# Kernel optimization log

Measured on AMD Instinct MI355X. Metric: run time of the kernel, lower is better.

## Reference

```python
import jax, jax.numpy as jnp
import numpy as np

B, H, M, K = 256, 1024, 20, 20  # batch, hidden, max_ingr, pairing top_k (must be equal: M==K)
VOCAB, INGR_V = 32000, 5000


def setup_inputs() -> dict:
    key = jax.random.key(0)
    ks = jax.random.split(key, 24)
    s = 0.02
    inp = {
        "input_ids": jax.random.randint(ks[0], (1, B), 0, VOCAB),
        "hidden": jax.random.normal(ks[1], (1, B, H), jnp.float32),
        "encoder_outputs": jax.random.normal(ks[2], (M, B, 2 * H), jnp.float32),
        "input_tensor": jax.random.randint(ks[3], (B, M), 0, INGR_V),
        "pairing_ids": jax.random.randint(ks[4], (INGR_V, K), 0, INGR_V),
        # parameters
        "emb_dec": jax.random.normal(ks[5], (VOCAB, H), jnp.float32) * s,
        "enc_emb": jax.random.normal(ks[6], (INGR_V, 2 * H), jnp.float32) * s,
        "Wq_i": jax.random.normal(ks[7], (H, H), jnp.float32) * s,
        "Wk_i": jax.random.normal(ks[8], (2 * H, H), jnp.float32) * s,
        "wa_i": jax.random.normal(ks[9], (H,), jnp.float32) * s,
        "Wq_p": jax.random.normal(ks[10], (H, H), jnp.float32) * s,
        "Wk_p": jax.random.normal(ks[11], (2 * H, H), jnp.float32) * s,
        "wa_p": jax.random.normal(ks[12], (H,), jnp.float32) * s,
        "ba_p": jax.random.normal(ks[13], (), jnp.float32) * s,
        "W_lin": jax.random.normal(ks[14], (3 * H, 2 * H), jnp.float32) * s,
        "b_lin": jnp.zeros((2 * H,), jnp.float32),
        "W_ih": jax.random.normal(ks[15], (3 * H, 2 * H), jnp.float32) * s,
        "W_hh": jax.random.normal(ks[16], (3 * H, H), jnp.float32) * s,
        "b_ih": jnp.zeros((3 * H,), jnp.float32),
        "b_hh": jnp.zeros((3 * H,), jnp.float32),
        "W_out": jax.random.normal(ks[17], (H, VOCAB), jnp.float32) * s,
        "b_out": jnp.zeros((VOCAB,), jnp.float32),
    }
    return inp


def reference(input_ids, hidden, encoder_outputs, input_tensor, pairing_ids,
              emb_dec, enc_emb, Wq_i, Wk_i, wa_i, Wq_p, Wk_p, wa_p, ba_p,
              W_lin, b_lin, W_ih, W_hh, b_ih, b_hh, W_out, b_out):
    h = hidden[0]                              # (B, H)
    emb = jnp.take(emb_dec, input_ids[0], axis=0)  # (B, H)

    # ---- IngrAtt (additive attention over ingredients) ----
    # torch code does a raw .view(B, M, 2H) on a (M, B, 2H) tensor -> plain reshape
    enc = encoder_outputs.reshape(B, M, 2 * H)
    query = h @ Wq_i                           # (B, H)
    key = enc @ Wk_i                           # (B, M, H)
    scores_i = jnp.tanh(query[:, None, :] + key) @ wa_i  # (B, M)
    aw = jax.nn.softmax(scores_i, axis=-1)     # (B, M)

    # ---- retrieval: pick most-attended ingredient, gather its top-k pairings ----
    ingr_arg = jnp.argmax(aw, axis=1)                          # (B,)
    ingr_id = input_tensor[jnp.arange(B), ingr_arg]            # (B,)
    comp_ids = jnp.take(pairing_ids, ingr_id, axis=0)          # (B, K)
    comp_emb = jnp.take(enc_emb, comp_ids, axis=0)             # (B, K, 2H)

    # ---- PairingAtt ----
    q_p = h @ Wq_p                             # (B, H)
    k_p = comp_emb @ Wk_p                      # (B, K, H)
    s_p = jnp.tanh(q_p[:, None, :] + k_p) @ wa_p + ba_p  # (B, K)
    a_p = jax.nn.softmax(s_p, axis=-1)
    attn_scores = a_p * s_p                    # (B, K) softmax-weighted raw scores
    attn_app = jnp.einsum('bk,bkd->bd', attn_scores, comp_emb)  # (B, 2H)

    out_pair = jnp.concatenate([emb, attn_app], axis=-1)  # (B, 3H)
    x = out_pair @ W_lin + b_lin                           # (B, 2H) -> GRU input

    # ---- single GRU step (torch gate ordering r,z,n) ----
    gi = x @ W_ih.T + b_ih
    gh = h @ W_hh.T + b_hh
    i_r, i_z, i_n = jnp.split(gi, 3, axis=-1)
    h_r, h_z, h_n = jnp.split(gh, 3, axis=-1)
    r = jax.nn.sigmoid(i_r + h_r)
    z = jax.nn.sigmoid(i_z + h_z)
    n = jnp.tanh(i_n + r * h_n)
    h_new = (1.0 - z) * n + z * h              # (B, H)

    logits = h_new @ W_out + b_out             # (B, VOCAB)
    return logits
```

## Files before the change

### kernel.cpp

```cpp
#include <hip/hip_runtime.h>
#include <cstdio>


using f32x4   = __attribute__((ext_vector_type(4))) float;
using bf16x8  = __attribute__((ext_vector_type(8))) short;
using ushort8 = __attribute__((ext_vector_type(8))) unsigned short;

__device__ __forceinline__ unsigned short f2bf(float x) {
    unsigned u = __builtin_bit_cast(unsigned, x);
    u += 0x7fffu + ((u >> 16) & 1u);
    return (unsigned short)(u >> 16);
}
__device__ __forceinline__ float bf2f(unsigned short u) {
    return __builtin_bit_cast(float, ((unsigned)u) << 16);
}

__device__ __forceinline__ void gload16(const void* g, void* l) {
    auto gp = (const __attribute__((address_space(1))) void*)g;
    auto lp = (__attribute__((address_space(3))) void*)l;
    __builtin_amdgcn_global_load_lds(gp, lp, 16, 0, 0);
}

__device__ __forceinline__ void transpose_body(
    const float* __restrict__ in, unsigned short* __restrict__ out,
    int R, int C, int r0, int c0)
{
    __shared__ float t[32][129];
    const int tid = threadIdx.x;
    const int lr = tid >> 3;
    const int cc = (tid & 7) * 4;
    #pragma unroll
    for (int i = 0; i < 4; ++i) {
        int r = lr + 32 * i;
        float4 v = *(const float4*)(in + (size_t)(r0 + r) * C + c0 + cc);
        t[cc + 0][r] = v.x; t[cc + 1][r] = v.y;
        t[cc + 2][r] = v.z; t[cc + 3][r] = v.w;
    }
    __syncthreads();
    const int rc = (tid & 15) * 8;
    #pragma unroll
    for (int p = 0; p < 2; ++p) {
        int c = (tid >> 4) + 16 * p;
        const float* src = &t[c][rc];
        ushort8 o;
        #pragma unroll
        for (int j = 0; j < 8; ++j) o[j] = f2bf(src[j]);
        *(ushort8*)(out + (size_t)(c0 + c) * R + r0 + rc) = o;
    }
}

__global__ __launch_bounds__(256) void prep1_kernel(
    const float* __restrict__ hidden, const float* __restrict__ enc_out,
    const float* __restrict__ enc_emb,
    const float* __restrict__ Wq_i, const float* __restrict__ Wq_p,
    const float* __restrict__ Wk_i, const float* __restrict__ Wk_p,
    unsigned short* __restrict__ hb, unsigned short* __restrict__ encb,
    unsigned short* __restrict__ encembb,
    unsigned short* __restrict__ WqiT, unsigned short* __restrict__ WqpT,
    unsigned short* __restrict__ WkiT, unsigned short* __restrict__ WkpT)
{
    const int bid = blockIdx.x;
    if (bid < 20496) {
        int i = bid * 256 + threadIdx.x;
        const float* src; unsigned short* dst; int j;
        if (i < 65536)        { src = hidden;  dst = hb;      j = i; }
        else if (i < 2686976) { src = enc_out; dst = encb;    j = i - 65536; }
        else                  { src = enc_emb; dst = encembb; j = i - 2686976; }
        float4 v = ((const float4*)src)[j];
        ((ushort4*)dst)[j] = make_ushort4(f2bf(v.x), f2bf(v.y), f2bf(v.z), f2bf(v.w));
    } else if (bid < 21008) {
        int local = bid - 20496;
        int bz = local >> 8, rem = local & 255;
        transpose_body(bz ? Wq_p : Wq_i, bz ? WqpT : WqiT,
                       1024, 1024, (rem >> 5) * 128, (rem & 31) * 32);
    } else {
        int local = bid - 21008;
        int bz = local >> 9, rem = local & 511;
        transpose_body(bz ? Wk_p : Wk_i, bz ? WkpT : WkiT,
                       2048, 1024, (rem >> 5) * 128, (rem & 31) * 32);
    }
}

template<int OUTBF, bool HAS_BIAS>
__device__ __forceinline__ void gemm_core(
    const unsigned short* __restrict__ A, const unsigned short* __restrict__ Bt,
    const float* __restrict__ bias, void* __restrict__ Cout, int Ncols,
    int sA, int sB, int kLen, int m0, int n0,
    unsigned short* lA, unsigned short* lB)
{
    const int tid = threadIdx.x;
    const int lane = tid & 63, wave = tid >> 6;
    const int wr = wave >> 1, wc = wave & 1;
    const int srow = tid >> 3, schunk = tid & 7;
    const int lm = lane & 15, lk = (lane >> 4) * 8;

    f32x4 acc[4][4];
    #pragma unroll
    for (int m = 0; m < 4; ++m)
        #pragma unroll
        for (int n = 0; n < 4; ++n) { f32x4 z = {0.f,0.f,0.f,0.f}; acc[m][n] = z; }

    const unsigned short* Ag = A  + (size_t)(m0 + srow) * sA + schunk * 8;
    const unsigned short* Bg = Bt + (size_t)(n0 + srow) * sB + schunk * 8;
    const int nt = kLen >> 6;

    char* lap = (char*)lA + tid * 16;
    char* lbp = (char*)lB + tid * 16;

    for (int t = 0; t < nt; ++t) {
        #pragma unroll
        for (int i = 0; i < 4; ++i) {
            gload16(Ag + (size_t)(32 * i) * sA + t * 64, lap + i * 4096);
            gload16(Bg + (size_t)(32 * i) * sB + t * 64, lbp + i * 4096);
        }
        __syncthreads();
        #pragma unroll
        for (int kk = 0; kk < 2; ++kk) {
            bf16x8 af[4], bv[4];
            #pragma unroll
            for (int m = 0; m < 4; ++m)
                af[m] = *(const bf16x8*)((const char*)lA +
                          (wr * 64 + m * 16 + lm) * 128 + (kk * 32 + lk) * 2);
            #pragma unroll
            for (int n = 0; n < 4; ++n)
                bv[n] = *(const bf16x8*)((const char*)lB +
                          (wc * 64 + n * 16 + lm) * 128 + (kk * 32 + lk) * 2);
            #pragma unroll
            for (int m = 0; m < 4; ++m)
                #pragma unroll
                for (int n = 0; n < 4; ++n)
                    acc[m][n] = __builtin_amdgcn_mfma_f32_16x16x32_bf16(
                        af[m], bv[n], acc[m][n], 0, 0, 0);
        }
        __syncthreads();
    }

    const int rbase = m0 + wr * 64 + (lane >> 4) * 4;
    const int cbase = n0 + wc * 64 + lm;
    #pragma unroll
    for (int m = 0; m < 4; ++m) {
        #pragma unroll
        for (int n = 0; n < 4; ++n) {
            int col = cbase + n * 16;
            float bvv = HAS_BIAS ? bias[col] : 0.0f;
            #pragma unroll
            for (int j = 0; j < 4; ++j) {
                int row = rbase + m * 16 + j;
                float v = acc[m][n][j] + bvv;
                if (OUTBF)
                    ((unsigned short*)Cout)[(size_t)row * Ncols + col] = f2bf(v);
                else
                    ((float*)Cout)[(size_t)row * Ncols + col] = v;
            }
        }
    }
}

#define GEMM_SHARED \
    __shared__ unsigned short lA[8192]; __shared__ unsigned short lB[8192];

__global__ __launch_bounds__(256) void gemm_dual_kernel(
    const unsigned short* A, const unsigned short* B0, const unsigned short* B1,
    float* P0, float* P1)
{
    GEMM_SHARED
    const int g = blockIdx.z >> 2, s = blockIdx.z & 3;
    const unsigned short* Bt = (g ? B1 : B0) + s * 256;
    float* C = (g ? P1 : P0) + (size_t)s * 262144;
    gemm_core<0,false>(A + s * 256, Bt, nullptr, C, 1024, 1024, 1024, 256,
                       blockIdx.y * 128, blockIdx.x * 128, lA, lB);
}

__global__ __launch_bounds__(256) void gemm24p_kernel(
    const unsigned short* encembb, const unsigned short* encb,
    const unsigned short* WkpT, const unsigned short* WkiT,
    unsigned short* kpP, unsigned short* keyP, size_t pStride)
{
    __shared__ unsigned short lA0[4096]; __shared__ unsigned short lA1[4096];
    __shared__ unsigned short lB0[4096]; __shared__ unsigned short lB1[4096];
    const int w   = (int)blockIdx.x;
    const int xcd = w & 7;
    const int r   = w >> 3;
    const int z   = xcd >> 1;
    const int by  = (xcd & 1) * 20 + (r >> 3);
    const int bx  = r & 7;
    const int g = z >> 1, h = z & 1;
    const unsigned short* A  = (g ? encb : encembb) + h * 1024;
    const unsigned short* Bt = (g ? WkiT : WkpT)    + h * 1024;
    unsigned short* Cb = (g ? keyP : kpP) + (size_t)h * pStride;
    const int m0 = by * 128, n0 = bx * 128;
    const int tid = threadIdx.x;
    const int lane = tid & 63, wave = tid >> 6;
    const int wr = wave >> 1, wc = wave & 1;
    const int lm = lane & 15;
    const int q  = lane >> 4;
    const int srow = tid >> 2;
    const int sc   = (tid & 3) ^ (srow & 3);

    f32x4 acc[4][4];
    #pragma unroll
    for (int m = 0; m < 4; ++m)
        #pragma unroll
        for (int n = 0; n < 4; ++n) { f32x4 zz = {0.f,0.f,0.f,0.f}; acc[m][n] = zz; }

    const unsigned short* Ag = A  + (size_t)(m0 + srow) * 2048 + sc * 8;
    const unsigned short* Bg = Bt + (size_t)(n0 + srow) * 2048 + sc * 8;

    auto stage = [&](unsigned short* la_, unsigned short* lb_, int t) {
        char* pa = (char*)la_ + tid * 16;
        char* pb = (char*)lb_ + tid * 16;
        gload16(Ag + t * 32, pa);
        gload16(Ag + (size_t)64 * 2048 + t * 32, pa + 4096);
        gload16(Bg + t * 32, pb);
        gload16(Bg + (size_t)64 * 2048 + t * 32, pb + 4096);
    };
    auto compute = [&](const unsigned short* la_, const unsigned short* lb_) {
        bf16x8 af[4], bv[4];
        #pragma unroll
        for (int m = 0; m < 4; ++m) {
            int rr = wr * 64 + m * 16 + lm;
            af[m] = *(const bf16x8*)((const char*)la_ + rr * 64 + ((q ^ (rr & 3)) * 16));
        }
        #pragma unroll
        for (int n = 0; n < 4; ++n) {
            int rr = wc * 64 + n * 16 + lm;
            bv[n] = *(const bf16x8*)((const char*)lb_ + rr * 64 + ((q ^ (rr & 3)) * 16));
        }
        #pragma unroll
        for (int m = 0; m < 4; ++m)
            #pragma unroll
            for (int n = 0; n < 4; ++n)
                acc[m][n] = __builtin_amdgcn_mfma_f32_16x16x32_bf16(
                    af[m], bv[n], acc[m][n], 0, 0, 0);
    };

    stage(lA0, lB0, 0);
    stage(lA1, lB1, 1);
    asm volatile("s_waitcnt vmcnt(4)" ::: "memory");
    __builtin_amdgcn_s_barrier();
    __builtin_amdgcn_sched_barrier(0);

    for (int t = 0; t < 30; t += 2) {
        compute(lA0, lB0);
        __builtin_amdgcn_s_barrier();
        __builtin_amdgcn_sched_barrier(0);
        stage(lA0, lB0, t + 2);
        asm volatile("s_waitcnt vmcnt(4)" ::: "memory");
        __builtin_amdgcn_s_barrier();
        __builtin_amdgcn_sched_barrier(0);

        compute(lA1, lB1);
        __builtin_amdgcn_s_barrier();
        __builtin_amdgcn_sched_barrier(0);
        stage(lA1, lB1, t + 3);
        asm volatile("s_waitcnt vmcnt(4)" ::: "memory");
        __builtin_amdgcn_s_barrier();
        __builtin_amdgcn_sched_barrier(0);
    }
    compute(lA0, lB0);
    asm volatile("s_waitcnt vmcnt(0)" ::: "memory");
    __builtin_amdgcn_s_barrier();
    __builtin_amdgcn_sched_barrier(0);
    compute(lA1, lB1);

    const int rbase = m0 + wr * 64 + q * 4;
    const int cbase = n0 + wc * 64 + lm;
    #pragma unroll
    for (int m = 0; m < 4; ++m)
        #pragma unroll
        for (int n = 0; n < 4; ++n)
            #pragma unroll
            for (int j = 0; j < 4; ++j)
                Cb[(size_t)(rbase + m * 16 + j) * 1024 + cbase + n * 16] =
                    f2bf(acc[m][n][j]);
}

__global__ __launch_bounds__(256) void attn_scores2q_kernel(
    const float* __restrict__ pqQ, const unsigned short* __restrict__ kP,
    size_t kStride, const float* __restrict__ wa, float* __restrict__ scores)
{
    const int bm = blockIdx.x;
    const int b  = bm / 20;
    const int tid = threadIdx.x;
    float4 qa = ((const float4*)(pqQ + (size_t)b * 1024))[tid];
    float4 qb = ((const float4*)(pqQ + 262144 + (size_t)b * 1024))[tid];
    float4 qc = ((const float4*)(pqQ + 524288 + (size_t)b * 1024))[tid];
    float4 qd = ((const float4*)(pqQ + 786432 + (size_t)b * 1024))[tid];
    float4 qv = make_float4(qa.x + qb.x + qc.x + qd.x, qa.y + qb.y + qc.y + qd.y,
                            qa.z + qb.z + qc.z + qd.z, qa.w + qb.w + qc.w + qd.w);
    ushort4 k0 = ((const ushort4*)(kP + (size_t)bm * 1024))[tid];
    ushort4 k1 = ((const ushort4*)(kP + kStride + (size_t)bm * 1024))[tid];
    float4 wv  = ((const float4*)wa)[tid];
    float p = tanhf(qv.x + bf2f(k0.x) + bf2f(k1.x)) * wv.x
            + tanhf(qv.y + bf2f(k0.y) + bf2f(k1.y)) * wv.y
            + tanhf(qv.z + bf2f(k0.z) + bf2f(k1.z)) * wv.z
            + tanhf(qv.w + bf2f(k0.w) + bf2f(k1.w)) * wv.w;
    #pragma unroll
    for (int off = 32; off > 0; off >>= 1) p += __shfl_down(p, off);
    __shared__ float sp[4];
    if ((tid & 63) == 0) sp[tid >> 6] = p;
    __syncthreads();
    if (tid == 0) scores[bm] = sp[0] + sp[1] + sp[2] + sp[3];
}

__device__ __forceinline__ int argmax_ing(
    const float* __restrict__ sc_i, const int* __restrict__ input_tensor, int b)
{
    float best = sc_i[b * 20]; int bi = 0;
    #pragma unroll
    for (int m = 1; m < 20; ++m) {
        float v = sc_i[b * 20 + m];
        if (v > best) { best = v; bi = m; }
    }
    return input_tensor[b * 20 + bi];
}

__global__ __launch_bounds__(256) void attn_scores_gather2q_kernel(
    const float* __restrict__ pqP, const unsigned short* __restrict__ kP,
    size_t kStride, const float* __restrict__ wa, const float* __restrict__ ba,
    const float* __restrict__ sc_i, const int* __restrict__ input_tensor,
    const int* __restrict__ pairing_ids, float* __restrict__ scores)
{
    const int bm = blockIdx.x;
    const int b  = bm / 20;
    const int kk = bm - b * 20;
    const int tid = threadIdx.x;
    const int ing = argmax_ing(sc_i, input_tensor, b);
    const int cid = pairing_ids[ing * 20 + kk];
    float4 qa = ((const float4*)(pqP + (size_t)b * 1024))[tid];
    float4 qb = ((const float4*)(pqP + 262144 + (size_t)b * 1024))[tid];
    float4 qc = ((const float4*)(pqP + 524288 + (size_t)b * 1024))[tid];
    float4 qd = ((const float4*)(pqP + 786432 + (size_t)b * 1024))[tid];
    float4 qv = make_float4(qa.x + qb.x + qc.x + qd.x, qa.y + qb.y + qc.y + qd.y,
                            qa.z + qb.z + qc.z + qd.z, qa.w + qb.w + qc.w + qd.w);
    ushort4 k0 = ((const ushort4*)(kP + (size_t)cid * 1024))[tid];
    ushort4 k1 = ((const ushort4*)(kP + kStride + (size_t)cid * 1024))[tid];
    float4 wv  = ((const float4*)wa)[tid];
    float p = tanhf(qv.x + bf2f(k0.x) + bf2f(k1.x)) * wv.x
            + tanhf(qv.y + bf2f(k0.y) + bf2f(k1.y)) * wv.y
            + tanhf(qv.z + bf2f(k0.z) + bf2f(k1.z)) * wv.z
            + tanhf(qv.w + bf2f(k0.w) + bf2f(k1.w)) * wv.w;
    #pragma unroll
    for (int off = 32; off > 0; off >>= 1) p += __shfl_down(p, off);
    __shared__ float sp[4];
    if ((tid & 63) == 0) sp[tid >> 6] = p;
    __syncthreads();
    if (tid == 0) scores[bm] = sp[0] + sp[1] + sp[2] + sp[3] + ba[0];
}

__global__ __launch_bounds__(256) void out_pair_kernel(
    const float* __restrict__ s_p, const float* __restrict__ enc_emb,
    const float* __restrict__ sc_i, const int* __restrict__ input_tensor,
    const int* __restrict__ pairing_ids,
    const float* __restrict__ emb_dec, const int* __restrict__ input_ids,
    unsigned short* __restrict__ out_pairb)
{
    const int b = blockIdx.x / 6, seg = blockIdx.x % 6;
    const int tid = threadIdx.x;
    const int d = seg * 512 + tid * 2;
    ushort2 o;
    if (seg < 2) {
        float2 v = *(const float2*)(emb_dec + (size_t)input_ids[b] * 1024 + d);
        o.x = f2bf(v.x); o.y = f2bf(v.y);
    } else {
        const int ing = argmax_ing(sc_i, input_tensor, b);
        __shared__ float s_raw[20];
        if (tid < 20) s_raw[tid] = s_p[b * 20 + tid];
        __syncthreads();
        float mx = -1e30f;
        #pragma unroll
        for (int m = 0; m < 20; ++m) mx = fmaxf(mx, s_raw[m]);
        float den = 0.f; float w[20];
        #pragma unroll
        for (int m = 0; m < 20; ++m) { w[m] = expf(s_raw[m] - mx); den += w[m]; }
        const float inv = 1.f / den;
        const int dd = d - 1024;
        float a0 = 0.f, a1 = 0.f;
        #pragma unroll
        for (int k = 0; k < 20; ++k) {
            const int cid = pairing_ids[ing * 20 + k];
            float2 v = *(const float2*)(enc_emb + (size_t)cid * 2048 + dd);
            float a = w[k] * inv * s_raw[k];
            a0 += a * v.x; a1 += a * v.y;
        }
        o.x = f2bf(a0); o.y = f2bf(a1);
    }
    *(ushort2*)(out_pairb + (size_t)b * 3072 + d) = o;
}

__global__ __launch_bounds__(256) void gemm5f_kernel(
    const unsigned short* __restrict__ A, const float* __restrict__ Wlin,
    float* __restrict__ P)
{
    __shared__ unsigned short lA[8192];
    __shared__ unsigned short lB[8192];
    const int tid = threadIdx.x;
    const int lane = tid & 63, wave = tid >> 6;
    const int wr = wave >> 1, wc = wave & 1;
    const int m0 = blockIdx.y * 128, n0 = blockIdx.x * 128;
    const int koff = blockIdx.z * 192;
    const int srow = tid >> 3, schunk = tid & 7;
    const int lm = lane & 15, lk = (lane >> 4) * 8;
    const int bcol = tid & 127, bkg = tid >> 7;
    const int bsw  = (bcol & 7) << 4;

    f32x4 acc[4][4];
    #pragma unroll
    for (int m = 0; m < 4; ++m)
        #pragma unroll
        for (int n = 0; n < 4; ++n) { f32x4 z = {0.f,0.f,0.f,0.f}; acc[m][n] = z; }

    const unsigned short* Ag = A + (size_t)(m0 + srow) * 3072 + koff + schunk * 8;
    char* lap = (char*)lA + tid * 16;

    for (int t = 0; t < 3; ++t) {
        #pragma unroll
        for (int i = 0; i < 4; ++i)
            gload16(Ag + (size_t)(32 * i) * 3072 + t * 64, lap + i * 4096);
        #pragma unroll
        for (int hh = 0; hh < 2; ++hh) {
            const int kbase = koff + t * 64 + bkg * 32 + hh * 16;
            ushort8 o0, o1;
            #pragma unroll
            for (int j = 0; j < 8; ++j)
                o0[j] = f2bf(Wlin[(size_t)(kbase + j) * 2048 + n0 + bcol]);
            #pragma unroll
            for (int j = 0; j < 8; ++j)
                o1[j] = f2bf(Wlin[(size_t)(kbase + 8 + j) * 2048 + n0 + bcol]);
            char* base = (char*)lB + bcol * 128;
            *(ushort8*)(base + ((bkg * 64 + hh * 32)      ^ bsw)) = o0;
            *(ushort8*)(base + ((bkg * 64 + hh * 32 + 16) ^ bsw)) = o1;
        }
        __syncthreads();
        #pragma unroll
        for (int kk = 0; kk < 2; ++kk) {
            bf16x8 af[4], bv[4];
            #pragma unroll
            for (int m = 0; m < 4; ++m)
                af[m] = *(const bf16x8*)((const char*)lA +
                          (wr * 64 + m * 16 + lm) * 128 + (kk * 32 + lk) * 2);
            #pragma unroll
            for (int n = 0; n < 4; ++n) {
                int rr = wc * 64 + n * 16 + lm;
                bv[n] = *(const bf16x8*)((const char*)lB +
                          rr * 128 + (((kk * 32 + lk) * 2) ^ ((rr & 7) << 4)));
            }
            #pragma unroll
            for (int m = 0; m < 4; ++m)
                #pragma unroll
                for (int n = 0; n < 4; ++n)
                    acc[m][n] = __builtin_amdgcn_mfma_f32_16x16x32_bf16(
                        af[m], bv[n], acc[m][n], 0, 0, 0);
        }
        __syncthreads();
    }

    float* C = P + (size_t)blockIdx.z * 524288;
    const int rbase = m0 + wr * 64 + (lane >> 4) * 4;
    const int cbase = n0 + wc * 64 + lm;
    #pragma unroll
    for (int m = 0; m < 4; ++m)
        #pragma unroll
        for (int n = 0; n < 4; ++n)
            #pragma unroll
            for (int j = 0; j < 4; ++j)
                C[(size_t)(rbase + m * 16 + j) * 2048 + cbase + n * 16] = acc[m][n][j];
}

__global__ __launch_bounds__(256) void gemm67f_kernel(
    const unsigned short* __restrict__ xb, const unsigned short* __restrict__ hb,
    const float* __restrict__ Wih, const float* __restrict__ Whh,
    float* __restrict__ pg)
{
    __shared__ unsigned short lA[8192];
    __shared__ unsigned short lB[8192];
    const int tid = threadIdx.x;
    const int lane = tid & 63, wave = tid >> 6;
    const int wr = wave >> 1, wc = wave & 1;
    const int g = blockIdx.z >> 2, s = blockIdx.z & 3;
    const unsigned short* A = g ? hb : xb;
    const float* Bf = g ? Whh : Wih;
    const int sA   = g ? 1024 : 2048;
    const int koff = g ? s * 256 : s * 512;
    const int nt   = g ? 4 : 8;
    const int m0 = blockIdx.y * 128, n0 = blockIdx.x * 128;
    const int srow = tid >> 3, schunk = tid & 7;
    const int lm = lane & 15, lk = (lane >> 4) * 8;
    const int bsw = (srow & 7) << 4;

    f32x4 acc[4][4];
    #pragma unroll
    for (int m = 0; m < 4; ++m)
        #pragma unroll
        for (int n = 0; n < 4; ++n) { f32x4 z = {0.f,0.f,0.f,0.f}; acc[m][n] = z; }

    const unsigned short* Ag = A  + (size_t)(m0 + srow) * sA + koff + schunk * 8;
    const float*          Bg = Bf + (size_t)(n0 + srow) * sA + koff + schunk * 8;
    char* lap = (char*)lA + tid * 16;

    for (int t = 0; t < nt; ++t) {
        #pragma unroll
        for (int i = 0; i < 4; ++i)
            gload16(Ag + (size_t)(32 * i) * sA + t * 64, lap + i * 4096);
        #pragma unroll
        for (int i = 0; i < 4; ++i) {
            const float* src = Bg + (size_t)(32 * i) * sA + t * 64;
            float4 v0 = *(const float4*)(src);
            float4 v1 = *(const float4*)(src + 4);
            ushort8 o;
            o[0] = f2bf(v0.x); o[1] = f2bf(v0.y); o[2] = f2bf(v0.z); o[3] = f2bf(v0.w);
            o[4] = f2bf(v1.x); o[5] = f2bf(v1.y); o[6] = f2bf(v1.z); o[7] = f2bf(v1.w);
            *(ushort8*)((char*)lB + (srow + 32 * i) * 128 + ((schunk * 16) ^ bsw)) = o;
        }
        __syncthreads();
        #pragma unroll
        for (int kk = 0; kk < 2; ++kk) {
            bf16x8 af[4], bv[4];
            #pragma unroll
            for (int m = 0; m < 4; ++m)
                af[m] = *(const bf16x8*)((const char*)lA +
                          (wr * 64 + m * 16 + lm) * 128 + (kk * 32 + lk) * 2);
            #pragma unroll
            for (int n = 0; n < 4; ++n) {
                int rr = wc * 64 + n * 16 + lm;
                bv[n] = *(const bf16x8*)((const char*)lB +
                          rr * 128 + (((kk * 32 + lk) * 2) ^ ((rr & 7) << 4)));
            }
            #pragma unroll
            for (int m = 0; m < 4; ++m)
                #pragma unroll
                for (int n = 0; n < 4; ++n)
                    acc[m][n] = __builtin_amdgcn_mfma_f32_16x16x32_bf16(
                        af[m], bv[n], acc[m][n], 0, 0, 0);
        }
        __syncthreads();
    }

    float* C = pg + (size_t)blockIdx.z * 786432;
    const int rbase = m0 + wr * 64 + (lane >> 4) * 4;
    const int cbase = n0 + wc * 64 + lm;
    #pragma unroll
    for (int m = 0; m < 4; ++m)
        #pragma unroll
        for (int n = 0; n < 4; ++n)
            #pragma unroll
            for (int j = 0; j < 4; ++j)
                C[(size_t)(rbase + m * 16 + j) * 3072 + cbase + n * 16] = acc[m][n][j];
}

__global__ __launch_bounds__(256) void gemm8_kernel(
    const unsigned short* __restrict__ A, const float* __restrict__ Wout,
    const float* __restrict__ bias, float* __restrict__ C)
{
    __shared__ unsigned short lA0[16384]; __shared__ unsigned short lA1[16384];
    __shared__ unsigned short lB0[4096];  __shared__ unsigned short lB1[4096];
    const int tid  = threadIdx.x;
    const int lane = tid & 63, wave = tid >> 6;
    const int n0 = blockIdx.x * 64;
    const int lm = lane & 15, lk = (lane >> 4) * 8;
    const int srow = tid >> 3, schunk = tid & 7;
    const int bcol = tid & 63, bkg = tid >> 6;
    const int bsw  = (bcol & 7) << 4;

    f32x4 acc[4][4];
    #pragma unroll
    for (int m = 0; m < 4; ++m)
        #pragma unroll
        for (int n = 0; n < 4; ++n) { f32x4 z = {0.f,0.f,0.f,0.f}; acc[m][n] = z; }

    const unsigned short* Ag = A + (size_t)srow * 1024 + schunk * 8;

    auto stageA = [&](unsigned short* la_, int t) {
        char* la = (char*)la_ + tid * 16;
        #pragma unroll
        for (int i = 0; i < 8; ++i)
            gload16(Ag + (size_t)(32 * i) * 1024 + t * 64, la + i * 4096);
    };
    float bv_[16];
    auto loadB = [&](int t) {
        const float* src = Wout + (size_t)(t * 64 + bkg * 16) * 32000 + n0 + bcol;
        #pragma unroll
        for (int j = 0; j < 16; ++j) bv_[j] = src[(size_t)j * 32000];
    };
    auto writeB = [&](unsigned short* lb_) {
        ushort8 o0, o1;
        #pragma unroll
        for (int j = 0; j < 8; ++j) { o0[j] = f2bf(bv_[j]); o1[j] = f2bf(bv_[j + 8]); }
        char* base = (char*)lb_ + bcol * 128;
        *(ushort8*)(base + ((bkg * 32)      ^ bsw)) = o0;
        *(ushort8*)(base + ((bkg * 32 + 16) ^ bsw)) = o1;
    };
    auto compute = [&](const unsigned short* la_, const unsigned short* lb_) {
        #pragma unroll
        for (int kk = 0; kk < 2; ++kk) {
            bf16x8 af[4], bv[4];
            #pragma unroll
            for (int m = 0; m < 4; ++m)
                af[m] = *(const bf16x8*)((const char*)la_ +
                          (wave * 64 + m * 16 + lm) * 128 + (kk * 32 + lk) * 2);
            #pragma unroll
            for (int n = 0; n < 4; ++n) {
                int rr = n * 16 + lm;
                bv[n] = *(const bf16x8*)((const char*)lb_ +
                          rr * 128 + (((kk * 32 + lk) * 2) ^ ((rr & 7) << 4)));
            }
            #pragma unroll
            for (int m = 0; m < 4; ++m)
                #pragma unroll
                for (int n = 0; n < 4; ++n)
                    acc[m][n] = __builtin_amdgcn_mfma_f32_16x16x32_bf16(
                        af[m], bv[n], acc[m][n], 0, 0, 0);
        }
    };

    stageA(lA0, 0); loadB(0); writeB(lB0);
    __syncthreads();
    const int nt = 16;
    for (int t = 0; t < nt; t += 2) {
        if (t + 1 < nt) { stageA(lA1, t + 1); loadB(t + 1); }
        compute(lA0, lB0);
        if (t + 1 < nt) writeB(lB1);
        __syncthreads();
        if (t + 1 < nt) {
            if (t + 2 < nt) { stageA(lA0, t + 2); loadB(t + 2); }
            compute(lA1, lB1);
            if (t + 2 < nt) writeB(lB0);
            __syncthreads();
        }
    }

    const int rbase = wave * 64 + (lane >> 4) * 4;
    const int cbase = n0 + lm;
    #pragma unroll
    for (int m = 0; m < 4; ++m) {
        #pragma unroll
        for (int n = 0; n < 4; ++n) {
            int col = cbase + n * 16;
            float bvv = bias[col];
            #pragma unroll
            for (int j = 0; j < 4; ++j)
                C[(size_t)(rbase + m * 16 + j) * 32000 + col] = acc[m][n][j] + bvv;
        }
    }
}

__global__ __launch_bounds__(256) void reduce5_kernel(
    const float* __restrict__ P, const float* __restrict__ bias,
    unsigned short* __restrict__ xb)
{
    int i = blockIdx.x * 256 + threadIdx.x;
    const float4* p = (const float4*)P;
    float4 bb = ((const float4*)bias)[i & 511];
    float s0 = bb.x, s1 = bb.y, s2 = bb.z, s3 = bb.w;
    #pragma unroll
    for (int s = 0; s < 16; ++s) {
        float4 v = p[i + s * 131072];
        s0 += v.x; s1 += v.y; s2 += v.z; s3 += v.w;
    }
    ((ushort4*)xb)[i] = make_ushort4(f2bf(s0), f2bf(s1), f2bf(s2), f2bf(s3));
}

__global__ __launch_bounds__(256) void gru_kernel(
    const float* __restrict__ pg, const float* __restrict__ b_ih,
    const float* __restrict__ b_hh, const float* __restrict__ h,
    unsigned short* __restrict__ hnewb)
{
    int idx = blockIdx.x * 256 + threadIdx.x;
    int b = idx >> 10, j = idx & 1023;
    float ir = b_ih[j], iz = b_ih[1024 + j], in_ = b_ih[2048 + j];
    float hr = b_hh[j], hz = b_hh[1024 + j], hn  = b_hh[2048 + j];
    #pragma unroll
    for (int s = 0; s < 4; ++s) {
        const float* gi = pg + (size_t)s * 786432 + (size_t)b * 3072;
        ir  += gi[j]; iz += gi[1024 + j]; in_ += gi[2048 + j];
        const float* gh = pg + (size_t)(4 + s) * 786432 + (size_t)b * 3072;
        hr  += gh[j]; hz += gh[1024 + j]; hn  += gh[2048 + j];
    }
    float r = 1.f / (1.f + expf(-(ir + hr)));
    float z = 1.f / (1.f + expf(-(iz + hz)));
    float n = tanhf(in_ + r * hn);
    hnewb[idx] = f2bf((1.f - z) * n + z * h[idx]);
}

extern "C" void kernel_launch(void* const* d_in, const int* in_sizes, int n_in,
                              void* d_out, int out_size, void* d_ws, size_t ws_size,
                              hipStream_t stream)
{
    const int*   input_ids    = (const int*)  d_in[0];
    const float* hidden       = (const float*)d_in[1];
    const float* enc_out      = (const float*)d_in[2];
    const int*   input_tensor = (const int*)  d_in[3];
    const int*   pairing_ids  = (const int*)  d_in[4];
    const float* emb_dec      = (const float*)d_in[5];
    const float* enc_emb      = (const float*)d_in[6];
    const float* Wq_i  = (const float*)d_in[7];
    const float* Wk_i  = (const float*)d_in[8];
    const float* wa_i  = (const float*)d_in[9];
    const float* Wq_p  = (const float*)d_in[10];
    const float* Wk_p  = (const float*)d_in[11];
    const float* wa_p  = (const float*)d_in[12];
    const float* ba_p  = (const float*)d_in[13];
    const float* W_lin = (const float*)d_in[14];
    const float* b_lin = (const float*)d_in[15];
    const float* W_ih  = (const float*)d_in[16];
    const float* W_hh  = (const float*)d_in[17];
    const float* b_ih  = (const float*)d_in[18];
    const float* b_hh  = (const float*)d_in[19];
    const float* W_out = (const float*)d_in[20];
    const float* b_out = (const float*)d_in[21];

    constexpr size_t OFF_HB    = 0;
    constexpr size_t OFF_HNEW  = 524288;
    constexpr size_t OFF_WQI   = 1048576;
    constexpr size_t OFF_WQP   = 3145728;
    constexpr size_t OFF_WKI   = 5242880;
    constexpr size_t OFF_WKP   = 9437184;
    constexpr size_t OFF_ENC   = 13631488;
    constexpr size_t OFF_SLOT1 = 34603008;
    constexpr size_t OFF_SLOT2 = 55574528;
    constexpr size_t OFF_SCI   = 78643200;
    constexpr size_t OFF_SCP   = 78667776;
    constexpr size_t OFF_PGI   = 1048576;
    constexpr size_t NEED      = 79167488;
    if (ws_size < NEED) {
        fprintf(stderr, "kernel_launch: ws_size %zu < needed %zu\n", ws_size, NEED);
        return;
    }
    char* ws = (char*)d_ws;
    unsigned short* hb     = (unsigned short*)(ws + OFF_HB);
    unsigned short* hnewb  = (unsigned short*)(ws + OFF_HNEW);
    unsigned short* WqiT   = (unsigned short*)(ws + OFF_WQI);
    unsigned short* WqpT   = (unsigned short*)(ws + OFF_WQP);
    unsigned short* WkiT   = (unsigned short*)(ws + OFF_WKI);
    unsigned short* WkpT   = (unsigned short*)(ws + OFF_WKP);
    unsigned short* encb   = (unsigned short*)(ws + OFF_ENC);
    unsigned short* kpP    = (unsigned short*)(ws + OFF_SLOT1);
    unsigned short* encembb= (unsigned short*)(ws + OFF_SLOT2);
    unsigned short* outp   = (unsigned short*)(ws + OFF_SLOT1);
    unsigned short* xb     = (unsigned short*)(ws + OFF_SLOT1 + 18350080);
    float*          sc_i   = (float*)         (ws + OFF_SCI);
    float*          sc_p   = (float*)         (ws + OFF_SCP);
    float*          pgi    = (float*)         (ws + OFF_PGI);
    unsigned short* keyP   = (unsigned short*)d_out;
    float*          pqQ    = (float*)((char*)d_out + 20971520);
    float*          pqP    = (float*)((char*)d_out + 20971520 + 4194304);
    float*          pG5    = (float*)d_out;

    constexpr size_t KP_STRIDE = 5120 * 1024;

    prep1_kernel<<<22032, 256, 0, stream>>>(hidden, enc_out, enc_emb,
                                            Wq_i, Wq_p, Wk_i, Wk_p,
                                            hb, encb, encembb,
                                            WqiT, WqpT, WkiT, WkpT);

    gemm_dual_kernel<<<dim3(8, 2, 8), 256, 0, stream>>>(hb, WqiT, WqpT, pqQ, pqP);

    gemm24p_kernel<<<1280, 256, 0, stream>>>(encembb, encb, WkpT, WkiT,
                                             kpP, keyP, KP_STRIDE);

    attn_scores2q_kernel<<<5120, 256, 0, stream>>>(pqQ, keyP, KP_STRIDE, wa_i, sc_i);
    attn_scores_gather2q_kernel<<<5120, 256, 0, stream>>>(pqP, kpP, KP_STRIDE, wa_p, ba_p,
                                                          sc_i, input_tensor, pairing_ids, sc_p);

    out_pair_kernel<<<1536, 256, 0, stream>>>(sc_p, enc_emb, sc_i, input_tensor,
                                              pairing_ids, emb_dec, input_ids, outp);

    gemm5f_kernel<<<dim3(16, 2, 16), 256, 0, stream>>>(outp, W_lin, pG5);
    reduce5_kernel<<<512, 256, 0, stream>>>(pG5, b_lin, xb);

    gemm67f_kernel<<<dim3(24, 2, 8), 256, 0, stream>>>(xb, hb, W_ih, W_hh, pgi);

    gru_kernel<<<1024, 256, 0, stream>>>(pgi, b_ih, b_hh, hidden, hnewb);

    gemm8_kernel<<<500, 256, 0, stream>>>(hnewb, W_out, b_out, (float*)d_out);
}
```

Measured before the change: 220.5 us.

## Drop split-K in key projection GEMM and use triple-buffered LDS pipeline

The key-projection GEMM previously split K=2048 into two halves, launched 1280 blocks and wrote two bf16 partial outputs that the score kernels summed. It now runs the full K per block with 640 blocks and a three-stage LDS buffer ring, writing a single bf16 result. This halves the output writes and the key reads in both attention score kernels, and removes one rounding of partials. The cost is half as many blocks (less parallelism on a 256-CU part) and more LDS per block, which may lower occupancy.

```diff
diff --git a/kernel.cpp b/kernel.cpp
--- a/kernel.cpp
+++ b/kernel.cpp
@@ -171,23 +171,24 @@
                        blockIdx.y * 128, blockIdx.x * 128, lA, lB);
 }
 
-__global__ __launch_bounds__(256) void gemm24p_kernel(
+__global__ __launch_bounds__(256) void gemm24p3_kernel(
     const unsigned short* encembb, const unsigned short* encb,
     const unsigned short* WkpT, const unsigned short* WkiT,
-    unsigned short* kpP, unsigned short* keyP, size_t pStride)
+    unsigned short* kp_all, unsigned short* key)
 {
     __shared__ unsigned short lA0[4096]; __shared__ unsigned short lA1[4096];
+    __shared__ unsigned short lA2[4096];
     __shared__ unsigned short lB0[4096]; __shared__ unsigned short lB1[4096];
+    __shared__ unsigned short lB2[4096];
     const int w   = (int)blockIdx.x;
     const int xcd = w & 7;
     const int r   = w >> 3;
-    const int z   = xcd >> 1;
-    const int by  = (xcd & 1) * 20 + (r >> 3);
+    const int g   = xcd >> 2;
+    const int by  = (xcd & 3) * 10 + (r >> 3);
     const int bx  = r & 7;
-    const int g = z >> 1, h = z & 1;
-    const unsigned short* A  = (g ? encb : encembb) + h * 1024;
-    const unsigned short* Bt = (g ? WkiT : WkpT)    + h * 1024;
-    unsigned short* Cb = (g ? keyP : kpP) + (size_t)h * pStride;
+    const unsigned short* A  = g ? encb : encembb;
+    const unsigned short* Bt = g ? WkiT : WkpT;
+    unsigned short* Cb = g ? key : kp_all;
     const int m0 = by * 128, n0 = bx * 128;
     const int tid = threadIdx.x;
     const int lane = tid & 63, wave = tid >> 6;
@@ -233,35 +234,48 @@
                 acc[m][n] = __builtin_amdgcn_mfma_f32_16x16x32_bf16(
                     af[m], bv[n], acc[m][n], 0, 0, 0);
     };
+    #define BAR() __builtin_amdgcn_s_barrier(); __builtin_amdgcn_sched_barrier(0)
+    #define WAIT8() asm volatile("s_waitcnt vmcnt(8)" ::: "memory")
 
     stage(lA0, lB0, 0);
     stage(lA1, lB1, 1);
+    stage(lA2, lB2, 2);
+    WAIT8();
+    BAR();
+
+    for (int t = 0; t < 60; t += 3) {
+        compute(lA0, lB0);
+        BAR();
+        stage(lA0, lB0, t + 3);
+        WAIT8();
+        BAR();
+
+        compute(lA1, lB1);
+        BAR();
+        stage(lA1, lB1, t + 4);
+        WAIT8();
+        BAR();
+
+        compute(lA2, lB2);
+        BAR();
+        stage(lA2, lB2, t + 5);
+        WAIT8();
+        BAR();
+    }
+    compute(lA0, lB0);
+    BAR();
+    stage(lA0, lB0, 63);
+    WAIT8();
+    BAR();
+    compute(lA1, lB1);
     asm volatile("s_waitcnt vmcnt(4)" ::: "memory");
-    __builtin_amdgcn_s_barrier();
-    __builtin_amdgcn_sched_barrier(0);
-
-    for (int t = 0; t < 30; t += 2) {
-        compute(lA0, lB0);
-        __builtin_amdgcn_s_barrier();
-        __builtin_amdgcn_sched_barrier(0);
-        stage(lA0, lB0, t + 2);
-        asm volatile("s_waitcnt vmcnt(4)" ::: "memory");
-        __builtin_amdgcn_s_barrier();
-        __builtin_amdgcn_sched_barrier(0);
-
-        compute(lA1, lB1);
-        __builtin_amdgcn_s_barrier();
-        __builtin_amdgcn_sched_barrier(0);
-        stage(lA1, lB1, t + 3);
-        asm volatile("s_waitcnt vmcnt(4)" ::: "memory");
-        __builtin_amdgcn_s_barrier();
-        __builtin_amdgcn_sched_barrier(0);
-    }
+    BAR();
+    compute(lA2, lB2);
+    asm volatile("s_waitcnt vmcnt(0)" ::: "memory");
+    BAR();
     compute(lA0, lB0);
-    asm volatile("s_waitcnt vmcnt(0)" ::: "memory");
-    __builtin_amdgcn_s_barrier();
-    __builtin_amdgcn_sched_barrier(0);
-    compute(lA1, lB1);
+    #undef BAR
+    #undef WAIT8
 
     const int rbase = m0 + wr * 64 + q * 4;
     const int cbase = n0 + wc * 64 + lm;
@@ -275,9 +289,9 @@
                     f2bf(acc[m][n][j]);
 }
 
-__global__ __launch_bounds__(256) void attn_scores2q_kernel(
-    const float* __restrict__ pqQ, const unsigned short* __restrict__ kP,
-    size_t kStride, const float* __restrict__ wa, float* __restrict__ scores)
+__global__ __launch_bounds__(256) void attn_scores_q_kernel(
+    const float* __restrict__ pqQ, const unsigned short* __restrict__ key,
+    const float* __restrict__ wa, float* __restrict__ scores)
 {
     const int bm = blockIdx.x;
     const int b  = bm / 20;
@@ -288,13 +302,10 @@
     float4 qd = ((const float4*)(pqQ + 786432 + (size_t)b * 1024))[tid];
     float4 qv = make_float4(qa.x + qb.x + qc.x + qd.x, qa.y + qb.y + qc.y + qd.y,
                             qa.z + qb.z + qc.z + qd.z, qa.w + qb.w + qc.w + qd.w);
-    ushort4 k0 = ((const ushort4*)(kP + (size_t)bm * 1024))[tid];
-    ushort4 k1 = ((const ushort4*)(kP + kStride + (size_t)bm * 1024))[tid];
+    ushort4 kv = ((const ushort4*)(key + (size_t)bm * 1024))[tid];
     float4 wv  = ((const float4*)wa)[tid];
-    float p = tanhf(qv.x + bf2f(k0.x) + bf2f(k1.x)) * wv.x
-            + tanhf(qv.y + bf2f(k0.y) + bf2f(k1.y)) * wv.y
-            + tanhf(qv.z + bf2f(k0.z) + bf2f(k1.z)) * wv.z
-            + tanhf(qv.w + bf2f(k0.w) + bf2f(k1.w)) * wv.w;
+    float p = tanhf(qv.x + bf2f(kv.x)) * wv.x + tanhf(qv.y + bf2f(kv.y)) * wv.y
+            + tanhf(qv.z + bf2f(kv.z)) * wv.z + tanhf(qv.w + bf2f(kv.w)) * wv.w;
     #pragma unroll
     for (int off = 32; off > 0; off >>= 1) p += __shfl_down(p, off);
     __shared__ float sp[4];
@@ -315,9 +326,9 @@
     return input_tensor[b * 20 + bi];
 }
 
-__global__ __launch_bounds__(256) void attn_scores_gather2q_kernel(
-    const float* __restrict__ pqP, const unsigned short* __restrict__ kP,
-    size_t kStride, const float* __restrict__ wa, const float* __restrict__ ba,
+__global__ __launch_bounds__(256) void attn_scores_gather_q_kernel(
+    const float* __restrict__ pqP, const unsigned short* __restrict__ kp_all,
+    const float* __restrict__ wa, const float* __restrict__ ba,
     const float* __restrict__ sc_i, const int* __restrict__ input_tensor,
     const int* __restrict__ pairing_ids, float* __restrict__ scores)
 {
@@ -333,13 +344,10 @@
     float4 qd = ((const float4*)(pqP + 786432 + (size_t)b * 1024))[tid];
     float4 qv = make_float4(qa.x + qb.x + qc.x + qd.x, qa.y + qb.y + qc.y + qd.y,
                             qa.z + qb.z + qc.z + qd.z, qa.w + qb.w + qc.w + qd.w);
-    ushort4 k0 = ((const ushort4*)(kP + (size_t)cid * 1024))[tid];
-    ushort4 k1 = ((const ushort4*)(kP + kStride + (size_t)cid * 1024))[tid];
+    ushort4 kv = ((const ushort4*)(kp_all + (size_t)cid * 1024))[tid];
     float4 wv  = ((const float4*)wa)[tid];
-    float p = tanhf(qv.x + bf2f(k0.x) + bf2f(k1.x)) * wv.x
-            + tanhf(qv.y + bf2f(k0.y) + bf2f(k1.y)) * wv.y
-            + tanhf(qv.z + bf2f(k0.z) + bf2f(k1.z)) * wv.z
-            + tanhf(qv.w + bf2f(k0.w) + bf2f(k1.w)) * wv.w;
+    float p = tanhf(qv.x + bf2f(kv.x)) * wv.x + tanhf(qv.y + bf2f(kv.y)) * wv.y
+            + tanhf(qv.z + bf2f(kv.z)) * wv.z + tanhf(qv.w + bf2f(kv.w)) * wv.w;
     #pragma unroll
     for (int off = 32; off > 0; off >>= 1) p += __shfl_down(p, off);
     __shared__ float sp[4];
@@ -734,19 +742,17 @@
     unsigned short* WkiT   = (unsigned short*)(ws + OFF_WKI);
     unsigned short* WkpT   = (unsigned short*)(ws + OFF_WKP);
     unsigned short* encb   = (unsigned short*)(ws + OFF_ENC);
-    unsigned short* kpP    = (unsigned short*)(ws + OFF_SLOT1);
+    unsigned short* kp_all = (unsigned short*)(ws + OFF_SLOT1);
     unsigned short* encembb= (unsigned short*)(ws + OFF_SLOT2);
     unsigned short* outp   = (unsigned short*)(ws + OFF_SLOT1);
     unsigned short* xb     = (unsigned short*)(ws + OFF_SLOT1 + 18350080);
     float*          sc_i   = (float*)         (ws + OFF_SCI);
     float*          sc_p   = (float*)         (ws + OFF_SCP);
     float*          pgi    = (float*)         (ws + OFF_PGI);
-    unsigned short* keyP   = (unsigned short*)d_out;
+    unsigned short* key    = (unsigned short*)d_out;
     float*          pqQ    = (float*)((char*)d_out + 20971520);
     float*          pqP    = (float*)((char*)d_out + 20971520 + 4194304);
     float*          pG5    = (float*)d_out;
-
-    constexpr size_t KP_STRIDE = 5120 * 1024;
 
     prep1_kernel<<<22032, 256, 0, stream>>>(hidden, enc_out, enc_emb,
                                             Wq_i, Wq_p, Wk_i, Wk_p,
@@ -755,12 +761,13 @@
 
     gemm_dual_kernel<<<dim3(8, 2, 8), 256, 0, stream>>>(hb, WqiT, WqpT, pqQ, pqP);
 
-    gemm24p_kernel<<<1280, 256, 0, stream>>>(encembb, encb, WkpT, WkiT,
-                                             kpP, keyP, KP_STRIDE);
-
-    attn_scores2q_kernel<<<5120, 256, 0, stream>>>(pqQ, keyP, KP_STRIDE, wa_i, sc_i);
-    attn_scores_gather2q_kernel<<<5120, 256, 0, stream>>>(pqP, kpP, KP_STRIDE, wa_p, ba_p,
-                                                          sc_i, input_tensor, pairing_ids, sc_p);
+    gemm24p3_kernel<<<640, 256, 0, stream>>>(encembb, encb, WkpT, WkiT,
+                                             kp_all, key);
+
+    attn_scores_q_kernel<<<5120, 256, 0, stream>>>(pqQ, key, wa_i, sc_i);
+    attn_scores_gather_q_kernel<<<5120, 256, 0, stream>>>(pqP, kp_all, wa_p, ba_p,
+                                                          sc_i, input_tensor,
+                                                          pairing_ids, sc_p);
 
     out_pair_kernel<<<1536, 256, 0, stream>>>(sc_p, enc_emb, sc_i, input_tensor,
                                               pairing_ids, emb_dec, input_ids, outp);
```

Result: slower. 233.7 us (+6.0%).
